# Performance work log

Hardware: AMD Instinct MI355X
Metric: run time of the kernel (lower is better)

Reference implementation:

```python
import jax, jax.numpy as jnp
import numpy as np

D_MODEL = 256
NHEAD = 8
NUM_EXPERTS = 5
LQ, LK, BATCH = 100, 1024, 16
LN_EPS = 1e-5


def setup_inputs() -> dict:
    key = jax.random.key(0)
    ks = jax.random.split(key, 12)
    d, E = D_MODEL, NUM_EXPERTS
    s = 1.0 / np.sqrt(d)
    return {
        "tgt": jax.random.normal(ks[0], (LQ, BATCH, d), jnp.float32),
        "memory": jax.random.normal(ks[1], (LK, BATCH, d), jnp.float32),
        "query_pos": jax.random.normal(ks[2], (LQ, BATCH, d), jnp.float32),
        "pos": jax.random.normal(ks[3], (LK, BATCH, d), jnp.float32),
        # per-expert MultiheadAttention params (packed q,k,v in_proj like torch)
        "w_in": jax.random.normal(ks[4], (E, 3 * d, d), jnp.float32) * s,
        "b_in": jnp.zeros((E, 3 * d), jnp.float32),
        "w_out": jax.random.normal(ks[5], (E, d, d), jnp.float32) * s,
        "b_out": jnp.zeros((E, d), jnp.float32),
        # gating network
        "w_gate": jax.random.normal(ks[6], (E, d), jnp.float32) * s,
        "b_gate": jnp.zeros((E,), jnp.float32),
        # LayerNorm
        "ln_gamma": jnp.ones((d,), jnp.float32),
        "ln_beta": jnp.zeros((d,), jnp.float32),
    }


def _moe_cross_attn(tgt, memory, query_pos, pos, w_in, b_in, w_out, b_out,
                    w_gate, b_gate, ln_gamma, ln_beta):
    Lq, B, d = tgt.shape
    H = NHEAD
    hd = d // H
    E = w_in.shape[0]
    Lk = memory.shape[0]

    # gating over (seq*batch, d) -> softmax over experts
    gate = jax.nn.softmax(tgt @ w_gate.T + b_gate, axis=-1)  # (Lq, B, E)

    q_emb = tgt + query_pos      # (Lq, B, d)
    k_emb = memory + pos         # (Lk, B, d)

    wq, wk, wv = w_in[:, :d], w_in[:, d:2 * d], w_in[:, 2 * d:]
    bq, bk, bv = b_in[:, :d], b_in[:, d:2 * d], b_in[:, 2 * d:]

    # batched projections across all experts (replaces python loop of MHA calls)
    q = jnp.einsum('lbd,eod->elbo', q_emb, wq) + bq[:, None, None, :]
    k = jnp.einsum('sbd,eod->esbo', k_emb, wk) + bk[:, None, None, :]
    v = jnp.einsum('sbd,eod->esbo', memory, wv) + bv[:, None, None, :]

    q = q.reshape(E, Lq, B, H, hd) * (1.0 / np.sqrt(hd))
    k = k.reshape(E, Lk, B, H, hd)
    v = v.reshape(E, Lk, B, H, hd)

    scores = jnp.einsum('elbhk,esbhk->ebhls', q, k)      # (E, B, H, Lq, Lk)
    attn = jax.nn.softmax(scores, axis=-1)
    ctx = jnp.einsum('ebhls,esbhk->elbhk', attn, v).reshape(E, Lq, B, d)

    out = jnp.einsum('elbd,eod->elbo', ctx, w_out) + b_out[:, None, None, :]

    # softmax-gated weighted combine of expert outputs
    mo = jnp.einsum('lbe,elbd->lbd', gate, out)

    x = tgt + mo  # dropout is identity (p=0.0)
    mu = jnp.mean(x, axis=-1, keepdims=True)
    var = jnp.var(x, axis=-1, keepdims=True)
    return (x - mu) * jax.lax.rsqrt(var + LN_EPS) * ln_gamma + ln_beta


def reference(tgt, memory, query_pos, pos, w_in, b_in, w_out, b_out,
              w_gate, b_gate, ln_gamma, ln_beta):
    return _moe_cross_attn(tgt, memory, query_pos, pos, w_in, b_in, w_out,
                           b_out, w_gate, b_gate, ln_gamma, ln_beta)
```

## Files before the change

### kernel.cpp

```cpp
#include <hip/hip_runtime.h>


typedef __bf16 bf16x8 __attribute__((ext_vector_type(8)));
typedef float f32x4 __attribute__((ext_vector_type(4)));
typedef unsigned int u32x4 __attribute__((ext_vector_type(4)));
typedef unsigned int u32x2 __attribute__((ext_vector_type(2)));
typedef unsigned short u16x4 __attribute__((ext_vector_type(4)));
typedef unsigned short us;

__device__ __forceinline__ us f2bf(float f) {
    unsigned u = __builtin_bit_cast(unsigned, f);
    u += 0x7FFFu + ((u >> 16) & 1u);
    return (us)(u >> 16);
}

__device__ __forceinline__ unsigned pack2(float lo, float hi) {
    return (unsigned)f2bf(lo) | ((unsigned)f2bf(hi) << 16);
}

__device__ __forceinline__ float bf2f(us v) {
    unsigned u = ((unsigned)v) << 16;
    return __builtin_bit_cast(float, u);
}

__device__ __forceinline__ bf16x8 ld_bf8(const us* p) {
    return __builtin_bit_cast(bf16x8, *reinterpret_cast<const u32x4*>(p));
}

__device__ __forceinline__ void gld_lds16(const us* g, us* l) {
    __builtin_amdgcn_global_load_lds(
        (const __attribute__((address_space(1))) unsigned int*)g,
        (__attribute__((address_space(3))) unsigned int*)l, 16, 0, 0);
}

__launch_bounds__(256)
__global__ void cvt_all(const float* __restrict__ tgt, const float* __restrict__ qpos,
                        const float* __restrict__ mem, const float* __restrict__ pos,
                        const float* __restrict__ w_in, const float* __restrict__ w_out,
                        const float* __restrict__ w_gate, const float* __restrict__ b_gate,
                        us* __restrict__ Aq, us* __restrict__ Ak, us* __restrict__ Av,
                        us* __restrict__ Wb, us* __restrict__ WOb,
                        float* __restrict__ Gate)
{
    const int bid = blockIdx.x;
    const int tid = threadIdx.x;
    if (bid < 400) {
        const int i = bid * 256 + tid;
        const int lane = tid & 63;
        const int row = i >> 6;
        f32x4 a = reinterpret_cast<const f32x4*>(tgt)[i];
        f32x4 b = reinterpret_cast<const f32x4*>(qpos)[i];
        u16x4 r;
#pragma unroll
        for (int j = 0; j < 4; ++j) r[j] = f2bf(a[j] + b[j]);
        reinterpret_cast<u16x4*>(Aq)[i] = r;
        float g[5];
#pragma unroll
        for (int e = 0; e < 5; ++e) {
            f32x4 wg = *reinterpret_cast<const f32x4*>(w_gate + e * 256 + 4 * lane);
            float p = a[0] * wg[0] + a[1] * wg[1] + a[2] * wg[2] + a[3] * wg[3];
#pragma unroll
            for (int off = 32; off >= 1; off >>= 1) p += __shfl_xor(p, off, 64);
            g[e] = p + b_gate[e];
        }
        float mx = g[0];
#pragma unroll
        for (int e = 1; e < 5; ++e) mx = fmaxf(mx, g[e]);
        float sm = 0.0f;
#pragma unroll
        for (int e = 0; e < 5; ++e) { g[e] = __expf(g[e] - mx); sm += g[e]; }
        const float invs = 1.0f / sm;
        if (lane == 0) {
#pragma unroll
            for (int e = 0; e < 5; ++e) Gate[row * 5 + e] = g[e] * invs;
        }
    } else if (bid < 4496) {
        int i = (bid - 400) * 256 + tid;
        f32x4 m = reinterpret_cast<const f32x4*>(mem)[i];
        f32x4 p = reinterpret_cast<const f32x4*>(pos)[i];
        u16x4 rk, rv;
#pragma unroll
        for (int j = 0; j < 4; ++j) { rk[j] = f2bf(m[j] + p[j]); rv[j] = f2bf(m[j]); }
        reinterpret_cast<u16x4*>(Ak)[i] = rk;
        reinterpret_cast<u16x4*>(Av)[i] = rv;
    } else if (bid < 5456) {
        int i = (bid - 4496) * 256 + tid;
        f32x4 a = reinterpret_cast<const f32x4*>(w_in)[i];
        u16x4 r;
#pragma unroll
        for (int j = 0; j < 4; ++j) r[j] = f2bf(a[j]);
        reinterpret_cast<u16x4*>(Wb)[i] = r;
    } else {
        int i = (bid - 5456) * 256 + tid;
        f32x4 a = reinterpret_cast<const f32x4*>(w_out)[i];
        u16x4 r;
#pragma unroll
        for (int j = 0; j < 4; ++j) r[j] = f2bf(a[j]);
        reinterpret_cast<u16x4*>(WOb)[i] = r;
    }
}

__launch_bounds__(256)
__global__ void gemm_qkv(const us* __restrict__ Aq, const us* __restrict__ Ak,
                         const us* __restrict__ Av, const us* __restrict__ Wb,
                         const float* __restrict__ b_in,
                         us* __restrict__ Qb, us* __restrict__ Kb, us* __restrict__ Vb)
{
    const int zr  = blockIdx.x;
    const int col0 = blockIdx.y * 128;
    const int rb  = blockIdx.z;
    const us* A; const us* W; const float* bias; us* C;
    float scale; int M;
    if (zr < 5) {
        if (rb >= 13) return;
        A = Aq; W = Wb + (size_t)zr * 196608; bias = b_in + (size_t)zr * 768;
        C = Qb + (size_t)zr * 409600; scale = 0.17677669529663687f; M = 1600;
    } else if (zr < 10) {
        const int e = zr - 5;
        A = Ak; W = Wb + 65536 + (size_t)e * 196608; bias = b_in + (size_t)e * 768 + 256;
        C = Kb + (size_t)e * 4194304; scale = 1.0f; M = 16384;
    } else {
        const int e = zr - 10;
        A = Av; W = Wb + 131072 + (size_t)e * 196608; bias = b_in + (size_t)e * 768 + 512;
        C = Vb + (size_t)e * 4194304; scale = 1.0f; M = 16384;
    }
    const int row0 = rb * 128;

    __shared__ us As[2 * 8192];
    const int tid  = threadIdx.x;
    const int lane = tid & 63;
    const int w    = tid >> 6;
    const int l15  = lane & 15;
    const int quad = lane >> 4;
    const int wm   = (w >> 1) * 64;
    const int wn   = (w & 1) * 64;
    const int srow = lane >> 3;
    const int gofs = ((lane & 7) ^ srow) * 8;

    auto stageA = [&](int buf, int kt) {
#pragma unroll
        for (int cc = 0; cc < 4; ++cc) {
            const int c = w * 4 + cc;
            gld_lds16(A + (size_t)(row0 + c * 8 + srow) * 256 + kt * 64 + gofs,
                      &As[buf * 8192 + c * 512]);
        }
    };

    f32x4 acc[4][4] = {};

    stageA(0, 0);

#pragma unroll
    for (int kt = 0; kt < 4; ++kt) {
        const int cur = kt & 1;
        u32x4 bf[2][4];
#pragma unroll
        for (int kh = 0; kh < 2; ++kh)
#pragma unroll
            for (int ni = 0; ni < 4; ++ni)
                bf[kh][ni] = *reinterpret_cast<const u32x4*>(
                    W + (size_t)(col0 + wn + ni * 16 + l15) * 256 + kt * 64 + kh * 32 + quad * 8);
        if (kt < 3) stageA(cur ^ 1, kt + 1);
        if (kt < 3) asm volatile("s_waitcnt vmcnt(4)" ::: "memory");
        else        asm volatile("s_waitcnt vmcnt(0)" ::: "memory");
        __builtin_amdgcn_s_barrier();
        __builtin_amdgcn_sched_barrier(0);
#pragma unroll
        for (int kh = 0; kh < 2; ++kh) {
            bf16x8 af[4];
#pragma unroll
            for (int mi = 0; mi < 4; ++mi) {
                const int row = wm + mi * 16 + l15;
                const int seg = (kh * 4 + quad) ^ (row & 7);
                af[mi] = ld_bf8(&As[cur * 8192 + row * 64 + seg * 8]);
            }
#pragma unroll
            for (int mi = 0; mi < 4; ++mi)
#pragma unroll
                for (int ni = 0; ni < 4; ++ni)
                    acc[mi][ni] = __builtin_amdgcn_mfma_f32_16x16x32_bf16(
                        __builtin_bit_cast(bf16x8, bf[kh][ni]), af[mi], acc[mi][ni], 0, 0, 0);
        }
        if (kt < 3) {
            asm volatile("s_waitcnt lgkmcnt(0)" ::: "memory");
            __builtin_amdgcn_sched_barrier(0);
            __builtin_amdgcn_s_barrier();
            __builtin_amdgcn_sched_barrier(0);
        }
    }

#pragma unroll
    for (int mi = 0; mi < 4; ++mi) {
        const int row = row0 + wm + mi * 16 + l15;
        if (row < M) {
#pragma unroll
            for (int ni = 0; ni < 4; ++ni) {
                const int colb = col0 + wn + ni * 16 + quad * 4;
                const f32x4 b4 = *reinterpret_cast<const f32x4*>(bias + colb);
                u32x2 pk;
                pk[0] = pack2((acc[mi][ni][0] + b4[0]) * scale,
                              (acc[mi][ni][1] + b4[1]) * scale);
                pk[1] = pack2((acc[mi][ni][2] + b4[2]) * scale,
                              (acc[mi][ni][3] + b4[3]) * scale);
                *reinterpret_cast<u32x2*>(C + (size_t)row * 256 + colb) = pk;
            }
        }
    }
}

__launch_bounds__(256)
__global__ void gemm_og(const us* __restrict__ PO, const float* __restrict__ PL,
                        const us* __restrict__ WOb, const float* __restrict__ b_out,
                        float* __restrict__ OUTf)
{
    const int e = blockIdx.z;
    const us* W = WOb + (size_t)e * 65536;
    const float* bias = b_out + (size_t)e * 256;
    float* Cout = OUTf + (size_t)e * 409600;

    const int row0 = blockIdx.x * 128;
    const int col0 = blockIdx.y * 128;
    __shared__ us As[2 * 8192];
    __shared__ us Bs[2 * 8192];
    const int tid  = threadIdx.x;
    const int lane = tid & 63;
    const int w    = tid >> 6;
    const int l15  = lane & 15;
    const int quad = lane >> 4;
    const int wm   = (w >> 1) * 64;
    const int wn   = (w & 1) * 64;
    const int srow = lane >> 3;
    const int gofs = ((lane & 7) ^ srow) * 8;

    u32x4 POr[4][4];
    float Lr[4];

    auto loadA = [&](int kt) {
#pragma unroll
        for (int cc = 0; cc < 4; ++cc) {
            const int c = w * 4 + cc;
            int grow = row0 + c * 8 + srow;
            if (grow > 1599) grow = 1599;
            const int d0 = kt * 64 + gofs;
            const size_t base = (size_t)e * 409600 + (size_t)grow * 256 + d0;
#pragma unroll
            for (int s = 0; s < 4; ++s)
                POr[cc][s] = *reinterpret_cast<const u32x4*>(PO + base + (size_t)s * 2048000);
            const int l = grow >> 4, bb = grow & 15, h = d0 >> 5;
            float L = 0.0f;
#pragma unroll
            for (int s = 0; s < 4; ++s)
                L += PL[((((size_t)s * 5 + e) * 16 + bb) * 8 + h) * 128 + l];
            Lr[cc] = L;
        }
    };
    auto writeA = [&](int buf) {
#pragma unroll
        for (int cc = 0; cc < 4; ++cc) {
            const float inv = 1.0f / Lr[cc];
            u32x4 pk;
#pragma unroll
            for (int j = 0; j < 4; ++j) {
                float v0 = 0.0f, v1 = 0.0f;
#pragma unroll
                for (int s = 0; s < 4; ++s) {
                    const unsigned u = POr[cc][s][j];
                    v0 += __builtin_bit_cast(float, u << 16);
                    v1 += __builtin_bit_cast(float, u & 0xffff0000u);
                }
                pk[j] = pack2(v0 * inv, v1 * inv);
            }
            *reinterpret_cast<u32x4*>(&As[buf * 8192 + (w * 4 + cc) * 512 + lane * 8]) = pk;
        }
    };
    auto loadW = [&](int buf, int kt) {
#pragma unroll
        for (int cc = 0; cc < 4; ++cc) {
            const int c = w * 4 + cc;
            const int row = c * 8 + srow;
            gld_lds16(W + (size_t)(col0 + row) * 256 + kt * 64 + gofs,
                      &Bs[buf * 8192 + c * 512]);
        }
    };

    loadA(0);
    loadW(0, 0);
    writeA(0);
    __syncthreads();

    f32x4 acc[4][4] = {};

#pragma unroll
    for (int kt = 0; kt < 4; ++kt) {
        const int cur = kt & 1;
        if (kt < 3) {
            loadA(kt + 1);
            loadW(cur ^ 1, kt + 1);
        }
#pragma unroll
        for (int kh = 0; kh < 2; ++kh) {
            bf16x8 af[4], bf[4];
#pragma unroll
            for (int mi = 0; mi < 4; ++mi) {
                const int row = wm + mi * 16 + l15;
                const int seg = (kh * 4 + quad) ^ (row & 7);
                af[mi] = ld_bf8(&As[cur * 8192 + row * 64 + seg * 8]);
            }
#pragma unroll
            for (int ni = 0; ni < 4; ++ni) {
                const int col = wn + ni * 16 + l15;
                const int seg = (kh * 4 + quad) ^ (col & 7);
                bf[ni] = ld_bf8(&Bs[cur * 8192 + col * 64 + seg * 8]);
            }
#pragma unroll
            for (int mi = 0; mi < 4; ++mi)
#pragma unroll
                for (int ni = 0; ni < 4; ++ni)
                    acc[mi][ni] = __builtin_amdgcn_mfma_f32_16x16x32_bf16(bf[ni], af[mi], acc[mi][ni], 0, 0, 0);
        }
        if (kt < 3) {
            writeA(cur ^ 1);
            __syncthreads();
        }
    }

#pragma unroll
    for (int mi = 0; mi < 4; ++mi) {
        const int row = row0 + wm + mi * 16 + l15;
        if (row < 1600) {
#pragma unroll
            for (int ni = 0; ni < 4; ++ni) {
                const int colb = col0 + wn + ni * 16 + quad * 4;
                const f32x4 b4 = *reinterpret_cast<const f32x4*>(bias + colb);
                f32x4 v;
#pragma unroll
                for (int r = 0; r < 4; ++r) v[r] = acc[mi][ni][r] + b4[r];
                *reinterpret_cast<f32x4*>(Cout + (size_t)row * 256 + colb) = v;
            }
        }
    }
}

__device__ __forceinline__ int vrow(int d) { return d * 264 + 8 * (d >> 3); }

__launch_bounds__(512)
__global__ void attn(const us* __restrict__ Qb, const us* __restrict__ Kb,
                     const us* __restrict__ Vb, us* __restrict__ PO,
                     float* __restrict__ PL)
{
    const int h = blockIdx.x;
    const int z = blockIdx.y;
    const int s = blockIdx.z;
    const int e = z >> 4, b = z & 15;
    const int tid  = threadIdx.x;
    const int w    = tid >> 6;
    const int lane = tid & 63;
    const int l15  = lane & 15, quad = lane >> 4;
    __shared__ us Ks[256 * 32];
    __shared__ us Vs[8464];
    __shared__ us Ps[7][16 * 40];

    const int key0 = s * 256;
    {
        const int kl  = lane >> 2;
        const int seg = lane & 3;
        const us* kg = Kb + ((size_t)((e * 1024 + key0 + w * 16 + kl) * 16 + b)) * 256
                          + h * 32 + seg * 8;
        gld_lds16(kg, &Ks[w * 512]);
        gld_lds16(kg + (size_t)128 * 16 * 256, &Ks[4096 + w * 512]);

        const int kv = tid >> 2;
        const int sg = tid & 3;
        const us* vg = Vb + ((size_t)((e * 1024 + key0 + kv) * 16 + b)) * 256
                          + h * 32 + sg * 8;
        u32x4 v0 = *reinterpret_cast<const u32x4*>(vg);
        u32x4 v1 = *reinterpret_cast<const u32x4*>(vg + (size_t)128 * 16 * 256);
#pragma unroll
        for (int j = 0; j < 4; ++j) {
            const int d0 = sg * 8 + 2 * j;
            const int e0 = vrow(d0);
            const int e1 = e0 + 264;
            Vs[e0 + kv]       = (us)(v0[j] & 0xffff);
            Vs[e1 + kv]       = (us)(v0[j] >> 16);
            Vs[e0 + 128 + kv] = (us)(v1[j] & 0xffff);
            Vs[e1 + 128 + kv] = (us)(v1[j] >> 16);
        }
    }
    u32x4 qraw = {0u, 0u, 0u, 0u};
    if (w < 7) {
        const int l = w * 16 + l15;
        if (l < 100)
            qraw = *reinterpret_cast<const u32x4*>(
                Qb + ((size_t)((e * 100 + l) * 16 + b)) * 256 + h * 32 + quad * 8);
    }
    const bf16x8 qf = __builtin_bit_cast(bf16x8, qraw);

    __syncthreads();

    if (w >= 7) return;

    const f32x4 zacc = {};
    f32x4 o0 = {}, o1 = {};
    float lsum = 0.0f;

    for (int c = 0; c < 8; ++c) {
        bf16x8 kf0 = ld_bf8(&Ks[(c * 32 + l15) * 32 + quad * 8]);
        bf16x8 kf1 = ld_bf8(&Ks[(c * 32 + 16 + l15) * 32 + quad * 8]);
        f32x4 s0 = __builtin_amdgcn_mfma_f32_16x16x32_bf16(kf0, qf, zacc, 0, 0, 0);
        f32x4 s1 = __builtin_amdgcn_mfma_f32_16x16x32_bf16(kf1, qf, zacc, 0, 0, 0);
        float p0[4], p1[4];
#pragma unroll
        for (int r = 0; r < 4; ++r) {
            p0[r] = __expf(s0[r]);
            p1[r] = __expf(s1[r]);
            lsum += p0[r] + p1[r];
        }
        u32x2 w0, w1;
        w0[0] = pack2(p0[0], p0[1]);
        w0[1] = pack2(p0[2], p0[3]);
        w1[0] = pack2(p1[0], p1[1]);
        w1[1] = pack2(p1[2], p1[3]);
        *reinterpret_cast<u32x2*>(&Ps[w][l15 * 40 + quad * 4])      = w0;
        *reinterpret_cast<u32x2*>(&Ps[w][l15 * 40 + 16 + quad * 4]) = w1;
        bf16x8 pf  = ld_bf8(&Ps[w][l15 * 40 + quad * 8]);
        bf16x8 vf0 = ld_bf8(&Vs[vrow(l15) + c * 32 + quad * 8]);
        bf16x8 vf1 = ld_bf8(&Vs[vrow(16 + l15) + c * 32 + quad * 8]);
        o0 = __builtin_amdgcn_mfma_f32_16x16x32_bf16(pf, vf0, o0, 0, 0, 0);
        o1 = __builtin_amdgcn_mfma_f32_16x16x32_bf16(pf, vf1, o1, 0, 0, 0);
    }

    lsum += __shfl_xor(lsum, 16, 64);
    lsum += __shfl_xor(lsum, 32, 64);

#pragma unroll
    for (int r = 0; r < 4; ++r) {
        const int row = w * 16 + quad * 4 + r;
        if (row < 100) {
            const size_t o = (((size_t)((s * 5 + e) * 100 + row)) * 16 + b) * 256 + h * 32;
            PO[o + l15]      = f2bf(o0[r]);
            PO[o + 16 + l15] = f2bf(o1[r]);
        }
    }
    const int q = w * 16 + l15;
    if (quad == 0 && q < 100)
        PL[((((size_t)s * 5 + e) * 16 + b) * 8 + h) * 128 + q] = lsum;
}

__launch_bounds__(256)
__global__ void finalize(const float* __restrict__ tgt, const float* __restrict__ Gate,
                         const float* __restrict__ OUTf,
                         const float* __restrict__ gamma, const float* __restrict__ beta,
                         float* __restrict__ out)
{
    const int row = blockIdx.x;
    const int d = threadIdx.x;
    __shared__ float red[8];
    const float t = tgt[(size_t)row * 256 + d];

    float mo = 0.0f;
#pragma unroll
    for (int e = 0; e < 5; ++e)
        mo += Gate[row * 5 + e] * OUTf[((size_t)e * 1600 + row) * 256 + d];
    const float x = t + mo;

    float p1 = x, p2 = x * x;
#pragma unroll
    for (int off = 32; off >= 1; off >>= 1) {
        p1 += __shfl_xor(p1, off, 64);
        p2 += __shfl_xor(p2, off, 64);
    }
    if ((d & 63) == 0) { red[d >> 6] = p1; red[4 + (d >> 6)] = p2; }
    __syncthreads();
    const float mean = (red[0] + red[1] + red[2] + red[3]) * (1.0f / 256.0f);
    const float msq  = (red[4] + red[5] + red[6] + red[7]) * (1.0f / 256.0f);
    const float var  = msq - mean * mean;

    out[(size_t)row * 256 + d] = (x - mean) * rsqrtf(var + 1e-5f) * gamma[d] + beta[d];
}

extern "C" void kernel_launch(void* const* d_in, const int* in_sizes, int n_in,
                              void* d_out, int out_size, void* d_ws, size_t ws_size,
                              hipStream_t stream)
{
    const float* tgt    = (const float*)d_in[0];
    const float* mem    = (const float*)d_in[1];
    const float* qpos   = (const float*)d_in[2];
    const float* pos    = (const float*)d_in[3];
    const float* w_in   = (const float*)d_in[4];
    const float* b_in   = (const float*)d_in[5];
    const float* w_out  = (const float*)d_in[6];
    const float* b_out  = (const float*)d_in[7];
    const float* w_gate = (const float*)d_in[8];
    const float* b_gate = (const float*)d_in[9];
    const float* ln_g   = (const float*)d_in[10];
    const float* ln_b   = (const float*)d_in[11];
    float* out = (float*)d_out;

    char* p = (char*)d_ws;
    auto alloc = [&](size_t n) { char* r = p; p += (n + 255) & ~(size_t)255; return r; };

    us* Aq   = (us*)alloc(409600ull * 2);
    us* Ak   = (us*)alloc(4194304ull * 2);
    us* Av   = (us*)alloc(4194304ull * 2);
    us* Wb   = (us*)alloc(983040ull * 2);
    us* WOb  = (us*)alloc(327680ull * 2);
    us* Qb   = (us*)alloc(5ull * 409600 * 2);
    us* Kb   = (us*)alloc(5ull * 4194304 * 2);
    us* Vb   = (us*)alloc(5ull * 4194304 * 2);
    float* OUTf  = (float*)alloc(5ull * 409600 * 4);
    float* Gate  = (float*)alloc(1600ull * 5 * 4);
    us*    PO = (us*)d_ws;
    float* PL = (float*)((char*)d_ws + 16384000);

    cvt_all<<<5776, 256, 0, stream>>>(tgt, qpos, mem, pos, w_in, w_out,
                                      w_gate, b_gate, Aq, Ak, Av, Wb, WOb, Gate);

    gemm_qkv<<<dim3(15, 2, 128), 256, 0, stream>>>(Aq, Ak, Av, Wb, b_in, Qb, Kb, Vb);

    attn<<<dim3(8, 80, 4), 512, 0, stream>>>(Qb, Kb, Vb, PO, PL);

    gemm_og<<<dim3(13, 2, 5), 256, 0, stream>>>(PO, PL, WOb, b_out, OUTf);

    finalize<<<1600, 256, 0, stream>>>(tgt, Gate, OUTf, ln_g, ln_b, out);
}
```

Before: 224.5 us.

## Deepen QKV GEMM prefetch to two stages and reorder grid for locality

Restructures the QKV projection GEMM main loop into an explicit two-deep software pipeline. Both the A tile (via LDS) and the W fragments (in registers, double-buffered) for the next k-step are issued before computing the current one, to hide global load latency. The grid is reordered so row blocks vary fastest, which groups blocks that share a weight slice in time for better cache reuse. It also adds a min-blocks-per-CU hint of 3. The extra register buffer raises register pressure, and the occupancy hint could force spills.

```diff
diff --git a/kernel.cpp b/kernel.cpp
--- a/kernel.cpp
+++ b/kernel.cpp
@@ -100,15 +100,15 @@
     }
 }
 
-__launch_bounds__(256)
+__launch_bounds__(256, 3)
 __global__ void gemm_qkv(const us* __restrict__ Aq, const us* __restrict__ Ak,
                          const us* __restrict__ Av, const us* __restrict__ Wb,
                          const float* __restrict__ b_in,
                          us* __restrict__ Qb, us* __restrict__ Kb, us* __restrict__ Vb)
 {
-    const int zr  = blockIdx.x;
+    const int rb   = blockIdx.x;
     const int col0 = blockIdx.y * 128;
-    const int rb  = blockIdx.z;
+    const int zr   = blockIdx.z;
     const us* A; const us* W; const float* bias; us* C;
     float scale; int M;
     if (zr < 5) {
@@ -145,26 +145,19 @@
                       &As[buf * 8192 + c * 512]);
         }
     };
+    auto loadW = [&](u32x4 (*dst)[4], int kt) {
+#pragma unroll
+        for (int kh = 0; kh < 2; ++kh)
+#pragma unroll
+            for (int ni = 0; ni < 4; ++ni)
+                dst[kh][ni] = *reinterpret_cast<const u32x4*>(
+                    W + (size_t)(col0 + wn + ni * 16 + l15) * 256 + kt * 64 + kh * 32 + quad * 8);
+    };
 
     f32x4 acc[4][4] = {};
-
-    stageA(0, 0);
-
-#pragma unroll
-    for (int kt = 0; kt < 4; ++kt) {
-        const int cur = kt & 1;
-        u32x4 bf[2][4];
-#pragma unroll
-        for (int kh = 0; kh < 2; ++kh)
-#pragma unroll
-            for (int ni = 0; ni < 4; ++ni)
-                bf[kh][ni] = *reinterpret_cast<const u32x4*>(
-                    W + (size_t)(col0 + wn + ni * 16 + l15) * 256 + kt * 64 + kh * 32 + quad * 8);
-        if (kt < 3) stageA(cur ^ 1, kt + 1);
-        if (kt < 3) asm volatile("s_waitcnt vmcnt(4)" ::: "memory");
-        else        asm volatile("s_waitcnt vmcnt(0)" ::: "memory");
-        __builtin_amdgcn_s_barrier();
-        __builtin_amdgcn_sched_barrier(0);
+    u32x4 bf0[2][4], bf1[2][4];
+
+    auto compute = [&](int cur, const u32x4 (*bq)[4]) {
 #pragma unroll
         for (int kh = 0; kh < 2; ++kh) {
             bf16x8 af[4];
@@ -179,15 +172,46 @@
 #pragma unroll
                 for (int ni = 0; ni < 4; ++ni)
                     acc[mi][ni] = __builtin_amdgcn_mfma_f32_16x16x32_bf16(
-                        __builtin_bit_cast(bf16x8, bf[kh][ni]), af[mi], acc[mi][ni], 0, 0, 0);
-        }
-        if (kt < 3) {
-            asm volatile("s_waitcnt lgkmcnt(0)" ::: "memory");
-            __builtin_amdgcn_sched_barrier(0);
-            __builtin_amdgcn_s_barrier();
-            __builtin_amdgcn_sched_barrier(0);
-        }
-    }
+                        __builtin_bit_cast(bf16x8, bq[kh][ni]), af[mi], acc[mi][ni], 0, 0, 0);
+        }
+    };
+
+    stageA(0, 0);  __builtin_amdgcn_sched_barrier(0);
+    loadW(bf0, 0); __builtin_amdgcn_sched_barrier(0);
+    stageA(1, 1);  __builtin_amdgcn_sched_barrier(0);
+    loadW(bf1, 1); __builtin_amdgcn_sched_barrier(0);
+
+    asm volatile("s_waitcnt vmcnt(12)" ::: "memory");
+    __builtin_amdgcn_s_barrier();
+    __builtin_amdgcn_sched_barrier(0);
+    compute(0, bf0);
+    asm volatile("s_waitcnt lgkmcnt(0)" ::: "memory");
+    __builtin_amdgcn_sched_barrier(0);
+    __builtin_amdgcn_s_barrier();
+    __builtin_amdgcn_sched_barrier(0);
+    stageA(0, 2);  __builtin_amdgcn_sched_barrier(0);
+    loadW(bf0, 2); __builtin_amdgcn_sched_barrier(0);
+
+    asm volatile("s_waitcnt vmcnt(12)" ::: "memory");
+    __builtin_amdgcn_s_barrier();
+    __builtin_amdgcn_sched_barrier(0);
+    compute(1, bf1);
+    asm volatile("s_waitcnt lgkmcnt(0)" ::: "memory");
+    __builtin_amdgcn_sched_barrier(0);
+    __builtin_amdgcn_s_barrier();
+    __builtin_amdgcn_sched_barrier(0);
+    stageA(1, 3);  __builtin_amdgcn_sched_barrier(0);
+    loadW(bf1, 3); __builtin_amdgcn_sched_barrier(0);
+
+    asm volatile("s_waitcnt vmcnt(12)" ::: "memory");
+    __builtin_amdgcn_s_barrier();
+    __builtin_amdgcn_sched_barrier(0);
+    compute(0, bf0);
+
+    asm volatile("s_waitcnt vmcnt(0)" ::: "memory");
+    __builtin_amdgcn_s_barrier();
+    __builtin_amdgcn_sched_barrier(0);
+    compute(1, bf1);
 
 #pragma unroll
     for (int mi = 0; mi < 4; ++mi) {
@@ -515,7 +539,7 @@
     cvt_all<<<5776, 256, 0, stream>>>(tgt, qpos, mem, pos, w_in, w_out,
                                       w_gate, b_gate, Aq, Ak, Av, Wb, WOb, Gate);
 
-    gemm_qkv<<<dim3(15, 2, 128), 256, 0, stream>>>(Aq, Ak, Av, Wb, b_in, Qb, Kb, Vb);
+    gemm_qkv<<<dim3(128, 2, 15), 256, 0, stream>>>(Aq, Ak, Av, Wb, b_in, Qb, Kb, Vb);
 
     attn<<<dim3(8, 80, 4), 512, 0, stream>>>(Qb, Kb, Vb, PO, PL);
 
```

After: 225.8 us. Within noise of the previous version (+0.5%).
